# Kernel optimization log

Hardware: AMD Instinct MI355X
Metric: run time of the kernel (lower is better)

## Reference

```python
import jax, jax.numpy as jnp
import numpy as np

HID = 128  # hidden_dim


def setup_inputs() -> dict:
    key = jax.random.key(0)
    ks = jax.random.split(key, 7)
    B, A, D, H, O = 256, 32, 128, HID, 128
    return {
        "h": jax.random.normal(ks[0], (B, A, D), dtype=jnp.float32),
        "message": jax.random.normal(ks[1], (B, A, A, D), dtype=jnp.float32),
        "mask": jax.random.randint(ks[2], (B, A, A), 0, 2, dtype=jnp.int32),
        "W": jax.random.normal(ks[3], (D, H), dtype=jnp.float32) * (1.0 / np.sqrt(H)),
        "a_w": jax.random.normal(ks[4], (2 * H,), dtype=jnp.float32) * 0.05,
        "out_w": jax.random.normal(ks[5], (O, H), dtype=jnp.float32) * 0.05,
        "out_b": jax.random.normal(ks[6], (O,), dtype=jnp.float32) * 0.05,
    }


def reference(h, message, mask, W, a_w, out_w, out_b):
    m = mask.astype(h.dtype)                      # [B,A,A]
    hW = jnp.matmul(h, W)                         # [B,A,H]
    Hm = jnp.matmul(message, W)                   # [B,A,A,H]
    # a(cat(h_repeat, H)) == h_repeat @ a_w[:H] + H @ a_w[H:] (avoids materializing concat)
    a1, a2 = a_w[:HID], a_w[HID:]
    E = jnp.einsum('bah,h->ba', hW, a1)[:, :, None] + jnp.einsum('bnah,h->bna', Hm, a2)  # [B,A,A]
    E = jnp.where(E >= 0, E, 0.2 * E)             # LeakyReLU(0.2)
    E_mask = E * m
    alpha = jax.nn.softmax(E_mask[..., None], axis=-2)   # softmax over dim=-2 (second agent dim)
    alpha_mask = jnp.nan_to_num(alpha * m[..., None])
    weighted_sum = jnp.sum(alpha_mask * Hm, axis=-2)      # [B,A,H]
    out = jnp.matmul(hW + weighted_sum, out_w.T) + out_b  # out_attn Linear
    return jax.nn.elu(out)
```

## Files before the change

### kernel.cpp

```cpp
#include <hip/hip_runtime.h>
#include <cstdint>
#include <cstddef>

#define HID 128
#define A_DIM 32


__global__ __launch_bounds__(256) void wa_kernel(const float* __restrict__ W,
                                                 const float* __restrict__ a_w,
                                                 float* __restrict__ ws) {
    const int tid = threadIdx.x;
    const int s = blockIdx.x * 32 + (tid >> 3);
    const int p8 = tid & 7;
    const int row = s & 127, which = s >> 7;
    const float4* W4 = reinterpret_cast<const float4*>(W);
    const float4* av = reinterpret_cast<const float4*>(a_w + which * HID);
    float p = 0.f;
#pragma unroll
    for (int i = 0; i < 4; ++i) {
        float4 wv = W4[row * 32 + p8 * 4 + i];
        float4 va = av[p8 * 4 + i];
        p += wv.x * va.x + wv.y * va.y + wv.z * va.z + wv.w * va.w;
    }
    p += __shfl_down(p, 4);
    p += __shfl_down(p, 2);
    p += __shfl_down(p, 1);
    if (p8 == 0) ws[s] = p;
}

__global__ __launch_bounds__(256, 4) void attn_kernel(
    const float* __restrict__ hmat,
    const float* __restrict__ message,
    const int* __restrict__ mask,
    const float* __restrict__ W,
    const float* __restrict__ out_w,
    float* __restrict__ ws,
    float* __restrict__ U) {
    const int tid = threadIdx.x;

    if (blockIdx.x < 64) {
        const int g = blockIdx.x * 256 + tid;
        const int d = g >> 7, o = g & 127;
        const float4* W4 = reinterpret_cast<const float4*>(W);
        const float4* ow4 = reinterpret_cast<const float4*>(out_w);
        float p = 0.f;
#pragma unroll 8
        for (int j = 0; j < 32; ++j) {
            float4 wv = W4[d * 32 + j];
            float4 ov = ow4[o * 32 + j];
            p += wv.x * ov.x + wv.y * ov.y + wv.z * ov.z + wv.w * ov.w;
        }
        ws[256 + d * HID + o] = p;
        return;
    }

    __shared__ float red[4][A_DIM][33];
    __shared__ float cf[4][A_DIM];

    const int w = tid >> 6;
    const int lane = tid & 63;
    const int half = lane >> 5;
    const int q = lane & 31;
    const size_t bid = (size_t)(blockIdx.x - 64) * 4 + w;

    const float4* gm4 = reinterpret_cast<const float4*>(message) + bid * (A_DIM * HID / 4);
    float4 v[16];
#pragma unroll
    for (int i = 0; i < 16; ++i) v[i] = gm4[(2 * i + half) * 32 + q];
    const float4* ws4 = reinterpret_cast<const float4*>(ws);
    float4 w1 = ws4[q];
    float4 w2 = ws4[32 + q];
    float4 h4 = (reinterpret_cast<const float4*>(hmat) + bid * 32)[q];
    float mv = (float)mask[bid * A_DIM + q];

    float pe1 = (half == 0) ? (h4.x * w1.x + h4.y * w1.y + h4.z * w1.z + h4.w * w1.w) : 0.f;
#pragma unroll
    for (int m = 32; m >= 1; m >>= 1) pe1 += __shfl_xor(pe1, m);

#pragma unroll
    for (int i = 0; i < 16; ++i) {
        float p2 = v[i].x * w2.x + v[i].y * w2.y + v[i].z * w2.z + v[i].w * w2.w;
        red[w][2 * i + half][q] = p2;
    }
    float e2 = 0.f;
#pragma unroll
    for (int k = 0; k < 16; ++k) e2 += red[w][q][16 * half + k];
    e2 += __shfl_xor(e2, 32);

    float e = pe1 + e2;
    e = (e >= 0.f) ? e : 0.2f * e;
    e *= mv;
    float mx = e;
#pragma unroll
    for (int m = 16; m >= 1; m >>= 1) mx = fmaxf(mx, __shfl_xor(mx, m));
    float ex = __expf(e - mx);
    float sum = ex;
#pragma unroll
    for (int m = 16; m >= 1; m >>= 1) sum += __shfl_xor(sum, m);
    float coef = ex / sum * mv;
    cf[w][q] = coef;

    float4 acc = {0.f, 0.f, 0.f, 0.f};
#pragma unroll
    for (int i = 0; i < 16; ++i) {
        float c = cf[w][2 * i + half];
        acc.x += c * v[i].x;
        acc.y += c * v[i].y;
        acc.z += c * v[i].z;
        acc.w += c * v[i].w;
    }
    acc.x += __shfl_xor(acc.x, 32);
    acc.y += __shfl_xor(acc.y, 32);
    acc.z += __shfl_xor(acc.z, 32);
    acc.w += __shfl_xor(acc.w, 32);

    if (half == 0) {
        float4 u;
        u.x = h4.x + acc.x;
        u.y = h4.y + acc.y;
        u.z = h4.z + acc.z;
        u.w = h4.w + acc.w;
        reinterpret_cast<float4*>(U)[bid * 32 + q] = u;
    }
}

__global__ __launch_bounds__(256) void out_kernel(
    const float* __restrict__ U,
    const float* __restrict__ ws,
    const float* __restrict__ out_b,
    float* __restrict__ out) {
    const float* P = ws + 256;
    __shared__ float u_lds[16][132];

    const int tid = threadIdx.x;
    const size_t row0 = (size_t)blockIdx.x * 16;
    const float4* gu = reinterpret_cast<const float4*>(U + row0 * HID);
#pragma unroll
    for (int i = 0; i < 2; ++i) {
        int idx = tid + i * 256;
        int r = idx >> 5, c4 = idx & 31;
        float4 vv = gu[idx];
        *reinterpret_cast<float4*>(&u_lds[r][c4 * 4]) = vv;
    }
    __syncthreads();

    const int tx = tid & 31;
    const int ty = tid >> 5;
    const float4* P4 = reinterpret_cast<const float4*>(P);

    float4 a0 = {0.f, 0.f, 0.f, 0.f}, a1 = {0.f, 0.f, 0.f, 0.f};
    for (int kg = 0; kg < 32; ++kg) {
        float4 p0 = P4[(4 * kg + 0) * 32 + tx];
        float4 p1 = P4[(4 * kg + 1) * 32 + tx];
        float4 p2 = P4[(4 * kg + 2) * 32 + tx];
        float4 p3 = P4[(4 * kg + 3) * 32 + tx];
        float4 u0 = *reinterpret_cast<const float4*>(&u_lds[2 * ty][4 * kg]);
        float4 u1 = *reinterpret_cast<const float4*>(&u_lds[2 * ty + 1][4 * kg]);
        a0.x += u0.x * p0.x + u0.y * p1.x + u0.z * p2.x + u0.w * p3.x;
        a0.y += u0.x * p0.y + u0.y * p1.y + u0.z * p2.y + u0.w * p3.y;
        a0.z += u0.x * p0.z + u0.y * p1.z + u0.z * p2.z + u0.w * p3.z;
        a0.w += u0.x * p0.w + u0.y * p1.w + u0.z * p2.w + u0.w * p3.w;
        a1.x += u1.x * p0.x + u1.y * p1.x + u1.z * p2.x + u1.w * p3.x;
        a1.y += u1.x * p0.y + u1.y * p1.y + u1.z * p2.y + u1.w * p3.y;
        a1.z += u1.x * p0.z + u1.y * p1.z + u1.z * p2.z + u1.w * p3.z;
        a1.w += u1.x * p0.w + u1.y * p1.w + u1.z * p2.w + u1.w * p3.w;
    }
    float4 b4 = reinterpret_cast<const float4*>(out_b)[tx];
    float4 o0, o1;
    float x;
    x = a0.x + b4.x; o0.x = (x > 0.f) ? x : expm1f(x);
    x = a0.y + b4.y; o0.y = (x > 0.f) ? x : expm1f(x);
    x = a0.z + b4.z; o0.z = (x > 0.f) ? x : expm1f(x);
    x = a0.w + b4.w; o0.w = (x > 0.f) ? x : expm1f(x);
    x = a1.x + b4.x; o1.x = (x > 0.f) ? x : expm1f(x);
    x = a1.y + b4.y; o1.y = (x > 0.f) ? x : expm1f(x);
    x = a1.z + b4.z; o1.z = (x > 0.f) ? x : expm1f(x);
    x = a1.w + b4.w; o1.w = (x > 0.f) ? x : expm1f(x);
    float4* out4 = reinterpret_cast<float4*>(out);
    out4[(row0 + 2 * ty) * 32 + tx] = o0;
    out4[(row0 + 2 * ty + 1) * 32 + tx] = o1;
}

extern "C" void kernel_launch(void* const* d_in, const int* in_sizes, int n_in,
                              void* d_out, int out_size, void* d_ws, size_t ws_size,
                              hipStream_t stream) {
    const float* hmat = (const float*)d_in[0];
    const float* message = (const float*)d_in[1];
    const int* mask = (const int*)d_in[2];
    const float* W = (const float*)d_in[3];
    const float* a_w = (const float*)d_in[4];
    const float* out_w = (const float*)d_in[5];
    const float* out_b = (const float*)d_in[6];
    float* out = (float*)d_out;
    float* ws = (float*)d_ws;
    float* U = ws + 256 + HID * HID;

    wa_kernel<<<8, 256, 0, stream>>>(W, a_w, ws);
    attn_kernel<<<64 + 2048, 256, 0, stream>>>(hmat, message, mask, W, out_w, ws, U);
    out_kernel<<<512, 256, 0, stream>>>(U, ws, out_b, out);
}
```

Measured before the change: 45.00 us.

## Fuse output projection into attention kernel and merge weight prep kernels

Moves the W·out_wᵀ product and the W·a_w projections into a single prep kernel, so the attention kernel no longer depends on a side product computed by blocks in the same launch. The output linear layer and ELU are fused into the attention kernel through a per-block LDS buffer of four rows, which removes the U round trip through global memory and one launch. The projected weight matrix is stored transposed so each thread does contiguous float4 dot products. In exchange, each block rereads the full 64KB projection matrix from cache, and the occupancy hint drops from 4 to 3.

```diff
diff --git a/kernel.cpp b/kernel.cpp
--- a/kernel.cpp
+++ b/kernel.cpp
@@ -6,42 +6,15 @@
 #define A_DIM 32
 
 
-__global__ __launch_bounds__(256) void wa_kernel(const float* __restrict__ W,
-                                                 const float* __restrict__ a_w,
-                                                 float* __restrict__ ws) {
+__global__ __launch_bounds__(256) void prep_kernel(const float* __restrict__ W,
+                                                   const float* __restrict__ a_w,
+                                                   const float* __restrict__ out_w,
+                                                   float* __restrict__ ws) {
     const int tid = threadIdx.x;
-    const int s = blockIdx.x * 32 + (tid >> 3);
-    const int p8 = tid & 7;
-    const int row = s & 127, which = s >> 7;
     const float4* W4 = reinterpret_cast<const float4*>(W);
-    const float4* av = reinterpret_cast<const float4*>(a_w + which * HID);
-    float p = 0.f;
-#pragma unroll
-    for (int i = 0; i < 4; ++i) {
-        float4 wv = W4[row * 32 + p8 * 4 + i];
-        float4 va = av[p8 * 4 + i];
-        p += wv.x * va.x + wv.y * va.y + wv.z * va.z + wv.w * va.w;
-    }
-    p += __shfl_down(p, 4);
-    p += __shfl_down(p, 2);
-    p += __shfl_down(p, 1);
-    if (p8 == 0) ws[s] = p;
-}
-
-__global__ __launch_bounds__(256, 4) void attn_kernel(
-    const float* __restrict__ hmat,
-    const float* __restrict__ message,
-    const int* __restrict__ mask,
-    const float* __restrict__ W,
-    const float* __restrict__ out_w,
-    float* __restrict__ ws,
-    float* __restrict__ U) {
-    const int tid = threadIdx.x;
-
     if (blockIdx.x < 64) {
         const int g = blockIdx.x * 256 + tid;
-        const int d = g >> 7, o = g & 127;
-        const float4* W4 = reinterpret_cast<const float4*>(W);
+        const int o = g >> 7, d = g & 127;
         const float4* ow4 = reinterpret_cast<const float4*>(out_w);
         float p = 0.f;
 #pragma unroll 8
@@ -50,18 +23,38 @@
             float4 ov = ow4[o * 32 + j];
             p += wv.x * ov.x + wv.y * ov.y + wv.z * ov.z + wv.w * ov.w;
         }
-        ws[256 + d * HID + o] = p;
-        return;
+        ws[256 + o * HID + d] = p;
+    } else {
+        const int row = tid & 127, which = tid >> 7;
+        const float4* av = reinterpret_cast<const float4*>(a_w) + which * 32;
+        float s = 0.f;
+#pragma unroll 8
+        for (int j = 0; j < 32; ++j) {
+            float4 wv = W4[row * 32 + j];
+            float4 va = av[j];
+            s += wv.x * va.x + wv.y * va.y + wv.z * va.z + wv.w * va.w;
+        }
+        ws[tid] = s;
     }
+}
 
+__global__ __launch_bounds__(256, 3) void fused_kernel(
+    const float* __restrict__ hmat,
+    const float* __restrict__ message,
+    const int* __restrict__ mask,
+    const float* __restrict__ ws,
+    const float* __restrict__ out_b,
+    float* __restrict__ out) {
     __shared__ float red[4][A_DIM][33];
     __shared__ float cf[4][A_DIM];
+    __shared__ float u_lds[4][HID];
 
+    const int tid = threadIdx.x;
     const int w = tid >> 6;
     const int lane = tid & 63;
     const int half = lane >> 5;
     const int q = lane & 31;
-    const size_t bid = (size_t)(blockIdx.x - 64) * 4 + w;
+    const size_t bid = (size_t)blockIdx.x * 4 + w;
 
     const float4* gm4 = reinterpret_cast<const float4*>(message) + bid * (A_DIM * HID / 4);
     float4 v[16];
@@ -97,8 +90,7 @@
     float sum = ex;
 #pragma unroll
     for (int m = 16; m >= 1; m >>= 1) sum += __shfl_xor(sum, m);
-    float coef = ex / sum * mv;
-    cf[w][q] = coef;
+    cf[w][q] = ex / sum * mv;
 
     float4 acc = {0.f, 0.f, 0.f, 0.f};
 #pragma unroll
@@ -120,65 +112,29 @@
         u.y = h4.y + acc.y;
         u.z = h4.z + acc.z;
         u.w = h4.w + acc.w;
-        reinterpret_cast<float4*>(U)[bid * 32 + q] = u;
-    }
-}
-
-__global__ __launch_bounds__(256) void out_kernel(
-    const float* __restrict__ U,
-    const float* __restrict__ ws,
-    const float* __restrict__ out_b,
-    float* __restrict__ out) {
-    const float* P = ws + 256;
-    __shared__ float u_lds[16][132];
-
-    const int tid = threadIdx.x;
-    const size_t row0 = (size_t)blockIdx.x * 16;
-    const float4* gu = reinterpret_cast<const float4*>(U + row0 * HID);
-#pragma unroll
-    for (int i = 0; i < 2; ++i) {
-        int idx = tid + i * 256;
-        int r = idx >> 5, c4 = idx & 31;
-        float4 vv = gu[idx];
-        *reinterpret_cast<float4*>(&u_lds[r][c4 * 4]) = vv;
+        *reinterpret_cast<float4*>(&u_lds[w][4 * q]) = u;
     }
     __syncthreads();
 
-    const int tx = tid & 31;
-    const int ty = tid >> 5;
-    const float4* P4 = reinterpret_cast<const float4*>(P);
-
-    float4 a0 = {0.f, 0.f, 0.f, 0.f}, a1 = {0.f, 0.f, 0.f, 0.f};
-    for (int kg = 0; kg < 32; ++kg) {
-        float4 p0 = P4[(4 * kg + 0) * 32 + tx];
-        float4 p1 = P4[(4 * kg + 1) * 32 + tx];
-        float4 p2 = P4[(4 * kg + 2) * 32 + tx];
-        float4 p3 = P4[(4 * kg + 3) * 32 + tx];
-        float4 u0 = *reinterpret_cast<const float4*>(&u_lds[2 * ty][4 * kg]);
-        float4 u1 = *reinterpret_cast<const float4*>(&u_lds[2 * ty + 1][4 * kg]);
-        a0.x += u0.x * p0.x + u0.y * p1.x + u0.z * p2.x + u0.w * p3.x;
-        a0.y += u0.x * p0.y + u0.y * p1.y + u0.z * p2.y + u0.w * p3.y;
-        a0.z += u0.x * p0.z + u0.y * p1.z + u0.z * p2.z + u0.w * p3.z;
-        a0.w += u0.x * p0.w + u0.y * p1.w + u0.z * p2.w + u0.w * p3.w;
-        a1.x += u1.x * p0.x + u1.y * p1.x + u1.z * p2.x + u1.w * p3.x;
-        a1.y += u1.x * p0.y + u1.y * p1.y + u1.z * p2.y + u1.w * p3.y;
-        a1.z += u1.x * p0.z + u1.y * p1.z + u1.z * p2.z + u1.w * p3.z;
-        a1.w += u1.x * p0.w + u1.y * p1.w + u1.z * p2.w + u1.w * p3.w;
+    const int g2 = tid >> 7;
+    const int o = tid & 127;
+    const float4* PT4 = reinterpret_cast<const float4*>(ws + 256) + (size_t)o * 32;
+    const float4* u0 = reinterpret_cast<const float4*>(&u_lds[2 * g2][0]);
+    const float4* u1 = reinterpret_cast<const float4*>(&u_lds[2 * g2 + 1][0]);
+    float a0 = 0.f, a1 = 0.f;
+#pragma unroll 8
+    for (int k = 0; k < 32; ++k) {
+        float4 pt = PT4[k];
+        float4 x0 = u0[k];
+        float4 x1 = u1[k];
+        a0 += x0.x * pt.x + x0.y * pt.y + x0.z * pt.z + x0.w * pt.w;
+        a1 += x1.x * pt.x + x1.y * pt.y + x1.z * pt.z + x1.w * pt.w;
     }
-    float4 b4 = reinterpret_cast<const float4*>(out_b)[tx];
-    float4 o0, o1;
-    float x;
-    x = a0.x + b4.x; o0.x = (x > 0.f) ? x : expm1f(x);
-    x = a0.y + b4.y; o0.y = (x > 0.f) ? x : expm1f(x);
-    x = a0.z + b4.z; o0.z = (x > 0.f) ? x : expm1f(x);
-    x = a0.w + b4.w; o0.w = (x > 0.f) ? x : expm1f(x);
-    x = a1.x + b4.x; o1.x = (x > 0.f) ? x : expm1f(x);
-    x = a1.y + b4.y; o1.y = (x > 0.f) ? x : expm1f(x);
-    x = a1.z + b4.z; o1.z = (x > 0.f) ? x : expm1f(x);
-    x = a1.w + b4.w; o1.w = (x > 0.f) ? x : expm1f(x);
-    float4* out4 = reinterpret_cast<float4*>(out);
-    out4[(row0 + 2 * ty) * 32 + tx] = o0;
-    out4[(row0 + 2 * ty + 1) * 32 + tx] = o1;
+    const float b = out_b[o];
+    float x = a0 + b;
+    out[((size_t)blockIdx.x * 4 + 2 * g2) * HID + o] = (x > 0.f) ? x : expm1f(x);
+    x = a1 + b;
+    out[((size_t)blockIdx.x * 4 + 2 * g2 + 1) * HID + o] = (x > 0.f) ? x : expm1f(x);
 }
 
 extern "C" void kernel_launch(void* const* d_in, const int* in_sizes, int n_in,
@@ -193,9 +149,7 @@
     const float* out_b = (const float*)d_in[6];
     float* out = (float*)d_out;
     float* ws = (float*)d_ws;
-    float* U = ws + 256 + HID * HID;
 
-    wa_kernel<<<8, 256, 0, stream>>>(W, a_w, ws);
-    attn_kernel<<<64 + 2048, 256, 0, stream>>>(hmat, message, mask, W, out_w, ws, U);
-    out_kernel<<<512, 256, 0, stream>>>(U, ws, out_b, out);
+    prep_kernel<<<65, 256, 0, stream>>>(W, a_w, out_w, ws);
+    fused_kernel<<<2048, 256, 0, stream>>>(hmat, message, mask, ws, out_b, out);
 }
```

Result: slower. 58.33 us (+29.6%).
